# Performance work log

Hardware: AMD Instinct MI355X
Metric: run time of the kernel (lower is better)

The kernel has to match this reference:

```python
import jax, jax.numpy as jnp
import numpy as np

EPS = 1e-12  # matches torch F.normalize eps

def _l2norm(v, axis):
    n = jnp.linalg.norm(v, axis=axis, keepdims=True)
    return v / jnp.maximum(n, EPS)

def setup_inputs() -> dict:
    key = jax.random.key(0)
    k1, k2 = jax.random.split(key)
    x = jax.random.normal(k1, (16, 512, 64, 64), dtype=jnp.float32)
    mem = jax.random.normal(k2, (1024, 512), dtype=jnp.float32)
    memory = _l2norm(mem, axis=1)  # buffer initialized normalized, as in __init__
    return {"x": x, "memory": memory}

def reference(x, memory):
    B, C, H, W = x.shape
    feat = x.transpose(0, 2, 3, 1).reshape(-1, C)          # [N, C], N=B*H*W
    feat_norm = _l2norm(feat, axis=1)                       # [N, C]
    mem_norm = _l2norm(memory, axis=1)                      # [K, C]
    sim = feat_norm @ mem_norm.T                            # [N, K] cosine sims
    attn = jax.nn.softmax(sim, axis=1)                      # [N, K]
    recon = attn @ mem_norm                                 # [N, C]
    recon = recon.reshape(B, H, W, C).transpose(0, 3, 1, 2) # [B, C, H, W]
    match_map = attn.max(axis=1).reshape(B, H, W)           # [B, H, W]
    return recon, match_map
```

## Files before the change

kernel.cpp:

```cpp
#include <hip/hip_runtime.h>

#define C_DIM 512
#define K_MEM 1024

typedef __attribute__((ext_vector_type(8))) short short8;
typedef __attribute__((ext_vector_type(4))) float f32x4;
typedef __attribute__((ext_vector_type(16))) float f32x16;
typedef __attribute__((ext_vector_type(4))) unsigned int u32x4;

#define LGKM0()  asm volatile("s_waitcnt lgkmcnt(0)" ::: "memory")
#define VM0()    asm volatile("s_waitcnt vmcnt(0)" ::: "memory")
#define BAR()    { asm volatile("" ::: "memory"); __builtin_amdgcn_s_barrier(); asm volatile("" ::: "memory"); }
#define SCHED0() __builtin_amdgcn_sched_barrier(0)

#define GLOAD16(dst, addr, imm) \
    asm volatile("global_load_dwordx4 %0, %1, off offset:%c2" \
                 : "=v"(dst) : "v"(addr), "n"(imm))
#define WAITV(N) do { asm volatile("s_waitcnt vmcnt(%c0)" :: "n"(N) : "memory"); \
                      __builtin_amdgcn_sched_barrier(0); } while (0)

__device__ __forceinline__ unsigned short f2bf(float f) {
    unsigned int u = __builtin_bit_cast(unsigned int, f);
    unsigned int r = (u + 0x7fffu + ((u >> 16) & 1u)) >> 16;
    return (unsigned short)r;
}

__device__ __forceinline__ f32x4 mfma16(short8 a, short8 b, f32x4 c) {
    return __builtin_amdgcn_mfma_f32_16x16x32_bf16(a, b, c, 0, 0, 0);
}
__device__ __forceinline__ f32x16 mfma32(short8 a, short8 b, f32x16 c) {
    return __builtin_amdgcn_mfma_f32_32x32x16_bf16(a, b, c, 0, 0, 0);
}

__device__ __forceinline__ void gl_lds16(const void* g, void* l) {
    __builtin_amdgcn_global_load_lds(
        (const __attribute__((address_space(1))) unsigned int*)g,
        (__attribute__((address_space(3))) unsigned int*)l, 16, 0, 0);
}

__global__ __launch_bounds__(256)
void prep_norm(const float* __restrict__ mem, unsigned short* __restrict__ Mn) {
    int k = blockIdx.x, t = threadIdx.x;
    const float* row = mem + (size_t)k * C_DIM;
    float2 v = *reinterpret_cast<const float2*>(row + 2 * t);
    float ss = v.x * v.x + v.y * v.y;
#pragma unroll
    for (int off = 32; off >= 1; off >>= 1) ss += __shfl_xor(ss, off);
    __shared__ float wp[4];
    if ((t & 63) == 0) wp[t >> 6] = ss;
    __syncthreads();
    float tot = wp[0] + wp[1] + wp[2] + wp[3];
    float rn = 1.0f / fmaxf(sqrtf(tot), 1e-12f);
    unsigned int pk = (unsigned int)f2bf(v.x * rn) | ((unsigned int)f2bf(v.y * rn) << 16);
    *reinterpret_cast<unsigned int*>(Mn + (size_t)k * C_DIM + 2 * t) = pk;
}

__global__ __launch_bounds__(256)
void prep_transpose(const unsigned short* __restrict__ Mn, unsigned short* __restrict__ MnT) {
    __shared__ unsigned short tl[64][72];
    int t = threadIdx.x;
    int bk = blockIdx.x & 15, bc = blockIdx.x >> 4;
    int k0 = bk * 64, c0 = bc * 64;
    {
        int kr = t >> 2, gc = (t & 3) * 16;
        const u32x4* src = reinterpret_cast<const u32x4*>(Mn + (size_t)(k0 + kr) * C_DIM + c0 + gc);
        u32x4 a = src[0], b = src[1];
        *reinterpret_cast<u32x4*>(&tl[kr][gc]) = a;
        *reinterpret_cast<u32x4*>(&tl[kr][gc + 8]) = b;
    }
    __syncthreads();
    {
        int cr = t >> 2, gk = (t & 3) * 16;
        unsigned int ow[8];
#pragma unroll
        for (int j = 0; j < 8; ++j)
            ow[j] = (unsigned int)tl[gk + 2 * j][cr] | ((unsigned int)tl[gk + 2 * j + 1][cr] << 16);
        unsigned int* dst = reinterpret_cast<unsigned int*>(MnT + (size_t)(c0 + cr) * K_MEM + k0 + gk);
#pragma unroll
        for (int j = 0; j < 8; ++j) dst[j] = ow[j];
    }
}

__global__ __launch_bounds__(512)
void normx_kernel(const float* __restrict__ x, unsigned short* __restrict__ Fn) {
    __shared__ alignas(16) char FnB[65536];
    __shared__ float normpart[64][9];
    __shared__ float rnormS[64];
    const int t = threadIdx.x, bid = blockIdx.x;
    const int b = bid >> 6, h = bid & 63;
    const int lane = t & 63, wv = t >> 6;
    const int w = lane, cg = wv;
    const float* xp = x + (size_t)b * 2097152 + (size_t)(cg * 64) * 4096 + (size_t)h * 64 + w;
    float xv[64];
#pragma unroll
    for (int i = 0; i < 64; ++i) xv[i] = xp[(size_t)i * 4096];
    float ss = 0.f;
#pragma unroll
    for (int i = 0; i < 64; ++i) ss += xv[i] * xv[i];
    normpart[w][cg] = ss;
    __syncthreads();
    if (t < 64) {
        float s = 0.f;
#pragma unroll
        for (int j = 0; j < 8; ++j) s += normpart[t][j];
        rnormS[t] = 1.0f / fmaxf(sqrtf(s), 1e-12f);
    }
    __syncthreads();
    float rn = rnormS[w];
    char* fnrow = FnB + w * 1024;
#pragma unroll
    for (int j = 0; j < 8; ++j) {
        u32x4 pk4;
#pragma unroll
        for (int p = 0; p < 4; ++p) {
            float v0 = xv[j * 8 + 2 * p] * rn;
            float v1 = xv[j * 8 + 2 * p + 1] * rn;
            pk4[p] = (unsigned int)f2bf(v0) | ((unsigned int)f2bf(v1) << 16);
        }
        int gs = (cg * 8 + j) ^ (w & 31);
        *(u32x4*)(fnrow + (gs << 4)) = pk4;
    }
    __syncthreads();
    const int r = t >> 3;
    char* orow = (char*)(Fn + (size_t)(bid * 64 + r) * C_DIM);
#pragma unroll
    for (int p = 0; p < 8; ++p) {
        int gl = p * 8 + (t & 7);
        u32x4 v = *(const u32x4*)(FnB + r * 1024 + ((gl ^ (r & 31)) << 4));
        *(u32x4*)(orow + gl * 16) = v;
    }
}

__device__ __forceinline__ void stage64(const char* g0, int rowBytes, int kcol,
                                        char* ldsChunk, int j, int wv, int lane) {
    const int rloc = wv * 8 + (lane >> 3);
    const int rglob = j * 64 + rloc;
    const int gs = (lane & 7) ^ (rloc & 7);
    gl_lds16(g0 + (size_t)rglob * rowBytes + kcol + gs * 16, ldsChunk + wv * 1024);
}
#define FRAG(base, r, gk) (*(const short8*)((base) + (r) * 128 + ((((gk)) ^ ((r) & 7)) << 4)))

#define GEMM_KLOOP(NKT, ABYT, BBYT)                                                   \
    {                                                                                  \
        for (int j = 0; j < 4; ++j) stage64(Ag, ABYT, 0, LDSU + j * 8192, j, wv, lane); \
        for (int j = 0; j < 4; ++j) stage64(Bg, BBYT, 0, LDSU + 32768 + j * 8192, j, wv, lane); \
        VM0(); BAR();                                                                   \
    }                                                                                  \
    _Pragma("unroll 1")                                                                \
    for (int kt = 0; kt < (NKT); ++kt) {                                               \
        char* Asp = LDSU + (kt & 1) * 65536;                                           \
        char* Bsp = Asp + 32768;                                                       \
        char* Asn = LDSU + ((kt + 1) & 1) * 65536;                                     \
        char* Bsn = Asn + 32768;                                                       \
        const int kcoln = (kt + 1) * 128;                                              \
        _Pragma("unroll")                                                              \
        for (int s = 0; s < 2; ++s) {                                                  \
            short8 af[4], bfv[4];                                                      \
            if (s == 0 && kt + 1 < (NKT)) {                                            \
                _Pragma("unroll")                                                      \
                for (int j = 0; j < 4; ++j)                                            \
                    stage64(Ag, ABYT, kcoln, Asn + j * 8192, j, wv, lane);             \
            }                                                                          \
            _Pragma("unroll")                                                          \
            for (int i = 0; i < 4; ++i) bfv[i] = FRAG(Bsp, wn * 64 + i * 16 + l15, s * 4 + l4); \
            _Pragma("unroll")                                                          \
            for (int i = 0; i < 4; ++i) af[i] = FRAG(Asp, wm * 128 + i * 16 + l15, s * 4 + l4); \
            SCHED0();                                                                  \
            __builtin_amdgcn_s_setprio(1);                                             \
            _Pragma("unroll")                                                          \
            for (int mf = 0; mf < 4; ++mf)                                             \
                _Pragma("unroll")                                                      \
                for (int nf = 0; nf < 4; ++nf)                                         \
                    acc[mf][nf] = mfma16(af[mf], bfv[nf], acc[mf][nf]);                \
            __builtin_amdgcn_s_setprio(0);                                             \
            SCHED0();                                                                  \
            if (s == 0 && kt + 1 < (NKT)) {                                            \
                _Pragma("unroll")                                                      \
                for (int j = 0; j < 4; ++j)                                            \
                    stage64(Bg, BBYT, kcoln, Bsn + j * 8192, j, wv, lane);             \
            }                                                                          \
            _Pragma("unroll")                                                          \
            for (int i = 0; i < 4; ++i) af[i] = FRAG(Asp, wm * 128 + (4 + i) * 16 + l15, s * 4 + l4); \
            SCHED0();                                                                  \
            __builtin_amdgcn_s_setprio(1);                                             \
            _Pragma("unroll")                                                          \
            for (int mf = 0; mf < 4; ++mf)                                             \
                _Pragma("unroll")                                                      \
                for (int nf = 0; nf < 4; ++nf)                                         \
                    acc[4 + mf][nf] = mfma16(af[mf], bfv[nf], acc[4 + mf][nf]);        \
            __builtin_amdgcn_s_setprio(0);                                             \
            SCHED0();                                                                  \
        }                                                                              \
        if (kt + 1 < (NKT)) VM0();                                                     \
        BAR();                                                                         \
    }

__global__ __launch_bounds__(512)
__attribute__((amdgpu_waves_per_eu(2, 2)))
void gemm1_kernel(const unsigned short* __restrict__ Fn, const unsigned short* __restrict__ Mn,
                  unsigned short* __restrict__ P, float* __restrict__ Zp, float* __restrict__ Mp) {
    __shared__ alignas(16) char LDSU[135168];
    __shared__ float zS[256][4], zM[256][4];

    const int wg = (blockIdx.x & 7) * 128 + (blockIdx.x >> 3);
    const int mt = wg >> 2, ntile = wg & 3;
    const int m0 = mt * 256, n0 = ntile * 256;
    const int t = threadIdx.x, lane = t & 63, wv = t >> 6;
    const int wm = wv >> 2, wn = wv & 3;
    const int l15 = lane & 15, l4 = lane >> 4;

    const char* Ag = (const char*)Fn + (size_t)m0 * 1024;
    const char* Bg = (const char*)Mn + (size_t)n0 * 1024;

    f32x4 acc[8][4];
#pragma unroll
    for (int i = 0; i < 8; ++i)
#pragma unroll
        for (int j = 0; j < 4; ++j) acc[i][j] = (f32x4){0.f, 0.f, 0.f, 0.f};

    GEMM_KLOOP(8, 1024, 1024)

    char* Pscr = LDSU;
#pragma unroll
    for (int mf = 0; mf < 8; ++mf) {
        float zs[4] = {0.f, 0.f, 0.f, 0.f};
        float zm[4] = {0.f, 0.f, 0.f, 0.f};
#pragma unroll
        for (int nf = 0; nf < 4; ++nf) {
            const int col = wn * 64 + nf * 16 + l15;
#pragma unroll
            for (int r = 0; r < 4; ++r) {
                float e = __expf(acc[mf][nf][r]);
                zs[r] += e;
                zm[r] = fmaxf(zm[r], e);
                const int row = wm * 128 + mf * 16 + l4 * 4 + r;
                *(unsigned short*)(Pscr + row * 528 + col * 2) = f2bf(e);
            }
        }
#pragma unroll
        for (int off = 1; off < 16; off <<= 1)
#pragma unroll
            for (int r = 0; r < 4; ++r) {
                zs[r] += __shfl_xor(zs[r], off);
                zm[r] = fmaxf(zm[r], __shfl_xor(zm[r], off));
            }
        if (l15 == 0) {
#pragma unroll
            for (int r = 0; r < 4; ++r) {
                const int row = wm * 128 + mf * 16 + l4 * 4 + r;
                zS[row][wn] = zs[r];
                zM[row][wn] = zm[r];
            }
        }
    }
    LGKM0(); BAR();
    if (t < 256) {
        float zq = zS[t][0] + zS[t][1] + zS[t][2] + zS[t][3];
        float mq = fmaxf(fmaxf(zM[t][0], zM[t][1]), fmaxf(zM[t][2], zM[t][3]));
        Zp[(size_t)(m0 + t) * 4 + ntile] = zq;
        Mp[(size_t)(m0 + t) * 4 + ntile] = mq;
    }
#pragma unroll
    for (int p = 0; p < 8; ++p) {
        const int r = p * 32 + (t >> 4);
        const char* src = Pscr + r * 528 + (t & 15) * 32;
        char* dst = (char*)P + (size_t)(m0 + r) * 2048 + n0 * 2 + (t & 15) * 32;
        u32x4 v0 = *(const u32x4*)src;
        u32x4 v1 = *(const u32x4*)(src + 16);
        *(u32x4*)dst = v0;
        *(u32x4*)(dst + 16) = v1;
    }
}

__global__ __launch_bounds__(256)
void stats_kernel(const float* __restrict__ Zp, const float* __restrict__ Mp,
                  float* __restrict__ Zinv, float* __restrict__ match) {
    int i = blockIdx.x * 256 + threadIdx.x;
    f32x4 a = *(const f32x4*)(Zp + (size_t)i * 4);
    f32x4 c = *(const f32x4*)(Mp + (size_t)i * 4);
    float s = a[0] + a[1] + a[2] + a[3];
    float m = fmaxf(fmaxf(c[0], c[1]), fmaxf(c[2], c[3]));
    float zi = 1.0f / s;
    Zinv[i] = zi;
    match[i] = m * zi;
}

__global__ __launch_bounds__(512)
__attribute__((amdgpu_waves_per_eu(2, 2)))
void gemm2_kernel(const unsigned short* __restrict__ P, const unsigned short* __restrict__ MnT,
                  const float* __restrict__ Zinv, float* __restrict__ recon) {
    __shared__ alignas(16) char LDSU[131072];
    __shared__ float zinvS[256];

    const int wg = (blockIdx.x & 7) * 64 + (blockIdx.x >> 3);
    const int mt = wg >> 1, ntile = wg & 1;
    const int m0 = mt * 256, n0 = ntile * 256;
    const int t = threadIdx.x, lane = t & 63, wv = t >> 6;
    const int wm = wv >> 2, wn = wv & 3;
    const int l15 = lane & 15, l4 = lane >> 4;

    if (t < 256) zinvS[t] = Zinv[m0 + t];

    const char* Ag = (const char*)P + (size_t)m0 * 2048;
    const char* Bg = (const char*)MnT + (size_t)n0 * 2048;

    f32x4 acc[8][4];
#pragma unroll
    for (int i = 0; i < 8; ++i)
#pragma unroll
        for (int j = 0; j < 4; ++j) acc[i][j] = (f32x4){0.f, 0.f, 0.f, 0.f};

    GEMM_KLOOP(16, 2048, 2048)

    const int b = m0 >> 12;
    const int inb0 = m0 & 4095;
#pragma unroll
    for (int mf = 0; mf < 8; ++mf) {
        f32x4 zv = *(const f32x4*)(&zinvS[wm * 128 + mf * 16 + l4 * 4]);
#pragma unroll
        for (int nf = 0; nf < 4; ++nf) {
            f32x4 v = acc[mf][nf];
            v[0] *= zv[0]; v[1] *= zv[1]; v[2] *= zv[2]; v[3] *= zv[3];
            const int c = n0 + wn * 64 + nf * 16 + l15;
            const int inb = inb0 + wm * 128 + mf * 16 + l4 * 4;
            *(f32x4*)(recon + (size_t)b * 2097152 + (size_t)c * 4096 + inb) = v;
        }
    }
}

__global__ __launch_bounds__(512)
__attribute__((amdgpu_waves_per_eu(2, 2)))
void fused_attn(const float* __restrict__ x,
                const unsigned short* __restrict__ Mn,
                const unsigned short* __restrict__ MnT,
                float* __restrict__ recon,
                float* __restrict__ match) {
    __shared__ alignas(16) char FnB[65536];
    __shared__ alignas(16) char PldsB[2 * 32768];
    __shared__ float Zinv[64], rnormS[64];

    const int t = threadIdx.x;
    const int bid = blockIdx.x;
    const int b = bid >> 6, h = bid & 63;
    const int lane = t & 63, wv = t >> 6;
    const int l31 = lane & 31, l5 = lane >> 5;
    const int ko = wv;
    const int cb = wv * 64;

    {
        float* normpart = (float*)PldsB;
        const int w = lane, cg = wv;
        const float* xp = x + (size_t)b * 2097152 + (size_t)(cg * 64) * 4096 + (size_t)h * 64 + w;
        float xv[64];
#pragma unroll
        for (int i = 0; i < 64; ++i) xv[i] = xp[(size_t)i * 4096];
        float ss = 0.f;
#pragma unroll
        for (int i = 0; i < 64; ++i) ss += xv[i] * xv[i];
        normpart[w * 9 + cg] = ss;
        __syncthreads();
        if (t < 64) {
            float s = 0.f;
#pragma unroll
            for (int j = 0; j < 8; ++j) s += normpart[t * 9 + j];
            rnormS[t] = 1.0f / fmaxf(sqrtf(s), 1e-12f);
        }
        __syncthreads();
        float rn = rnormS[w];
        char* fnrow = FnB + w * 1024;
#pragma unroll
        for (int j = 0; j < 8; ++j) {
            u32x4 pk4;
#pragma unroll
            for (int p = 0; p < 4; ++p) {
                float v0 = xv[j * 8 + 2 * p] * rn;
                float v1 = xv[j * 8 + 2 * p + 1] * rn;
                pk4[p] = (unsigned int)f2bf(v0) | ((unsigned int)f2bf(v1) << 16);
            }
            int gs = (cg * 8 + j) ^ (w & 31);
            *(u32x4*)(fnrow + (gs << 4)) = pk4;
        }
    }
    __syncthreads();

    f32x16 acc3[2][2];
#pragma unroll
    for (int i = 0; i < 2; ++i)
#pragma unroll
        for (int j = 0; j < 2; ++j)
#pragma unroll
            for (int r = 0; r < 16; ++r) acc3[i][j][r] = 0.f;

    float regZ[2] = {0.f, 0.f};
    float regM[2] = {-3.0e38f, -3.0e38f};
    const char* fnR0 = FnB + l31 * 1024;
    const char* fnR1 = FnB + (32 + l31) * 1024;

#pragma unroll 1
    for (int kt = 0; kt < 4; ++kt) {
        const char* aG = (const char*)Mn + ((size_t)(kt * 256 + ko * 32 + l31) << 10) + (l5 << 4);
        u32x4 afb[2][4];
        GLOAD16(afb[0][0], aG, 0);
        GLOAD16(afb[0][1], aG, 32);
        GLOAD16(afb[0][2], aG, 64);
        GLOAD16(afb[0][3], aG, 96);
        f32x16 acc1[2];
#pragma unroll
        for (int j = 0; j < 2; ++j)
#pragma unroll
            for (int r = 0; r < 16; ++r) acc1[j][r] = 0.f;
#pragma unroll
        for (int g = 0; g < 8; ++g) {
            if (g < 7) {
#pragma unroll
                for (int s = 0; s < 4; ++s)
                    GLOAD16(afb[(g + 1) & 1][s], aG, ((g + 1) * 4 + s) * 32);
                WAITV(4);
            } else {
                WAITV(0);
            }
#pragma unroll
            for (int s = 0; s < 4; ++s) {
                const int st = g * 4 + s;
                const int gsw = (((st << 1) | l5) ^ l31) << 4;
                short8 b0 = *(const short8*)(fnR0 + gsw);
                short8 b1 = *(const short8*)(fnR1 + gsw);
                short8 av = __builtin_bit_cast(short8, afb[g & 1][s]);
                acc1[0] = mfma32(av, b0, acc1[0]);
                acc1[1] = mfma32(av, b1, acc1[1]);
            }
        }
        const char* aG2a = (const char*)MnT + ((size_t)(cb + l31) << 11) + ((size_t)kt << 9) + (l5 << 4);
        const char* aG2b = aG2a + 65536;
        u32x4 a2b[2][4];
        GLOAD16(a2b[0][0], aG2a, 0);
        GLOAD16(a2b[0][1], aG2b, 0);
        GLOAD16(a2b[0][2], aG2a, 32);
        GLOAD16(a2b[0][3], aG2b, 32);
        unsigned int P32[2][8];
#pragma unroll
        for (int nt = 0; nt < 2; ++nt) {
            float s0 = 0.f, m0 = -3.0e38f;
#pragma unroll
            for (int j = 0; j < 8; ++j) {
                float a0 = acc1[nt][2 * j], a1 = acc1[nt][2 * j + 1];
                m0 = fmaxf(m0, fmaxf(a0, a1));
                float e0 = __expf(a0), e1 = __expf(a1);
                P32[nt][j] = (unsigned int)f2bf(e0) | ((unsigned int)f2bf(e1) << 16);
                s0 += e0 + e1;
            }
            s0 += __shfl_xor(s0, 32);
            m0 = fmaxf(m0, __shfl_xor(m0, 32));
            regZ[nt] += s0;
            regM[nt] = fmaxf(regM[nt], m0);
        }
        char* Pb = PldsB + (kt & 1) * 32768;
#pragma unroll
        for (int nt = 0; nt < 2; ++nt) {
            const int n = nt * 32 + l31;
            char* prow = Pb + n * 512;
#pragma unroll
            for (int jp = 0; jp < 4; ++jp) {
                const int gk = ko * 4 + jp;
                uint2 v;
                v.x = P32[nt][2 * jp];
                v.y = P32[nt][2 * jp + 1];
                *(uint2*)(prow + ((gk ^ (n & 31)) << 4) + 8 * l5) = v;
            }
        }
        LGKM0(); BAR();
#pragma unroll
        for (int g = 0; g < 8; ++g) {
            if (g < 7) {
#pragma unroll
                for (int u = 0; u < 2; ++u) {
                    GLOAD16(a2b[(g + 1) & 1][u * 2 + 0], aG2a, ((g + 1) * 2 + u) * 32);
                    GLOAD16(a2b[(g + 1) & 1][u * 2 + 1], aG2b, ((g + 1) * 2 + u) * 32);
                }
                WAITV(4);
            } else {
                WAITV(0);
            }
#pragma unroll
            for (int u = 0; u < 2; ++u) {
                const int ks = g * 2 + u;
                const int gsw = (((ks << 1) | l5) ^ l31) << 4;
                short8 bp0 = *(const short8*)(Pb + l31 * 512 + gsw);
                short8 bp1 = *(const short8*)(Pb + (32 + l31) * 512 + gsw);
                short8 a0 = __builtin_bit_cast(short8, a2b[g & 1][u * 2 + 0]);
                short8 a1 = __builtin_bit_cast(short8, a2b[g & 1][u * 2 + 1]);
                acc3[0][0] = mfma32(a0, bp0, acc3[0][0]);
                acc3[0][1] = mfma32(a0, bp1, acc3[0][1]);
                acc3[1][0] = mfma32(a1, bp0, acc3[1][0]);
                acc3[1][1] = mfma32(a1, bp1, acc3[1][1]);
            }
        }
    }
    {
        float* pS = (float*)FnB;
        float* pM = (float*)(FnB + 2048);
        if (l5 == 0) {
            pS[ko * 64 + l31] = regZ[0];
            pS[ko * 64 + 32 + l31] = regZ[1];
            pM[ko * 64 + l31] = regM[0];
            pM[ko * 64 + 32 + l31] = regM[1];
        }
        LGKM0(); BAR();
        if (t < 64) {
            float s = 0.f, m = -3.0e38f;
#pragma unroll
            for (int k8 = 0; k8 < 8; ++k8) {
                s += pS[k8 * 64 + t];
                m = fmaxf(m, pM[k8 * 64 + t]);
            }
            float zi = 1.0f / s;
            Zinv[t] = zi;
            match[(size_t)bid * 64 + t] = __expf(m) * zi;
        }
        LGKM0(); BAR();
    }
    const float zi0 = Zinv[l31], zi1 = Zinv[32 + l31];
    float* rbase = recon + (size_t)b * 2097152 + (size_t)h * 64;
#pragma unroll
    for (int ct = 0; ct < 2; ++ct) {
#pragma unroll
        for (int r = 0; r < 16; ++r) {
            const int c = cb + ct * 32 + (r & 3) + 8 * (r >> 2) + 4 * l5;
            float* rp = rbase + (size_t)c * 4096;
            rp[l31] = acc3[ct][0][r] * zi0;
            rp[32 + l31] = acc3[ct][1][r] * zi1;
        }
    }
}

extern "C" void kernel_launch(void* const* d_in, const int* in_sizes, int n_in,
                              void* d_out, int out_size, void* d_ws, size_t ws_size,
                              hipStream_t stream) {
    (void)in_sizes; (void)n_in; (void)out_size;
    if (ws_size < (size_t)2 * 1024 * 1024) return;

    const float* x = (const float*)d_in[0];
    const float* mem = (const float*)d_in[1];
    float* recon = (float*)d_out;
    float* match = recon + (size_t)16 * 512 * 64 * 64;
    char* ws = (char*)d_ws;
    unsigned short* Mn = (unsigned short*)ws;
    unsigned short* MnT = (unsigned short*)(ws + 1048576);

    prep_norm<<<dim3(K_MEM), dim3(256), 0, stream>>>(mem, Mn);
    prep_transpose<<<dim3(128), dim3(256), 0, stream>>>(Mn, MnT);

    const size_t NEED = 205783040ull;
    if (ws_size >= NEED) {
        unsigned short* Fn = (unsigned short*)(ws + 2097152);
        unsigned short* P  = (unsigned short*)(ws + 69206016);
        float* Zp = (float*)(ws + 203423744);
        float* Mp = (float*)(ws + 204472320);
        float* Zi = (float*)(ws + 205520896);
        normx_kernel<<<dim3(1024), dim3(512), 0, stream>>>(x, Fn);
        gemm1_kernel<<<dim3(1024), dim3(512), 0, stream>>>(Fn, Mn, P, Zp, Mp);
        stats_kernel<<<dim3(256), dim3(256), 0, stream>>>(Zp, Mp, Zi, match);
        gemm2_kernel<<<dim3(512), dim3(512), 0, stream>>>(P, MnT, Zi, recon);
    } else {
        fused_attn<<<dim3(1024), dim3(512), 0, stream>>>(x, Mn, MnT, recon, match);
    }
}
```

Before: 276.7 us.

## Restructure GEMM k-loop into half-tile staged pipeline with partial vmcnt waits

```diff
diff --git a/kernel.cpp b/kernel.cpp
--- a/kernel.cpp
+++ b/kernel.cpp
@@ -131,69 +131,80 @@
     }
 }
 
-__device__ __forceinline__ void stage64(const char* g0, int rowBytes, int kcol,
-                                        char* ldsChunk, int j, int wv, int lane) {
-    const int rloc = wv * 8 + (lane >> 3);
-    const int rglob = j * 64 + rloc;
-    const int gs = (lane & 7) ^ (rloc & 7);
-    gl_lds16(g0 + (size_t)rglob * rowBytes + kcol + gs * 16, ldsChunk + wv * 1024);
-}
-#define FRAG(base, r, gk) (*(const short8*)((base) + (r) * 128 + ((((gk)) ^ ((r) & 7)) << 4)))
-
-#define GEMM_KLOOP(NKT, ABYT, BBYT)                                                   \
-    {                                                                                  \
-        for (int j = 0; j < 4; ++j) stage64(Ag, ABYT, 0, LDSU + j * 8192, j, wv, lane); \
-        for (int j = 0; j < 4; ++j) stage64(Bg, BBYT, 0, LDSU + 32768 + j * 8192, j, wv, lane); \
-        VM0(); BAR();                                                                   \
-    }                                                                                  \
-    _Pragma("unroll 1")                                                                \
-    for (int kt = 0; kt < (NKT); ++kt) {                                               \
-        char* Asp = LDSU + (kt & 1) * 65536;                                           \
-        char* Bsp = Asp + 32768;                                                       \
-        char* Asn = LDSU + ((kt + 1) & 1) * 65536;                                     \
-        char* Bsn = Asn + 32768;                                                       \
-        const int kcoln = (kt + 1) * 128;                                              \
-        _Pragma("unroll")                                                              \
-        for (int s = 0; s < 2; ++s) {                                                  \
-            short8 af[4], bfv[4];                                                      \
-            if (s == 0 && kt + 1 < (NKT)) {                                            \
-                _Pragma("unroll")                                                      \
-                for (int j = 0; j < 4; ++j)                                            \
-                    stage64(Ag, ABYT, kcoln, Asn + j * 8192, j, wv, lane);             \
-            }                                                                          \
-            _Pragma("unroll")                                                          \
-            for (int i = 0; i < 4; ++i) bfv[i] = FRAG(Bsp, wn * 64 + i * 16 + l15, s * 4 + l4); \
-            _Pragma("unroll")                                                          \
-            for (int i = 0; i < 4; ++i) af[i] = FRAG(Asp, wm * 128 + i * 16 + l15, s * 4 + l4); \
-            SCHED0();                                                                  \
-            __builtin_amdgcn_s_setprio(1);                                             \
-            _Pragma("unroll")                                                          \
-            for (int mf = 0; mf < 4; ++mf)                                             \
-                _Pragma("unroll")                                                      \
-                for (int nf = 0; nf < 4; ++nf)                                         \
-                    acc[mf][nf] = mfma16(af[mf], bfv[nf], acc[mf][nf]);                \
-            __builtin_amdgcn_s_setprio(0);                                             \
-            SCHED0();                                                                  \
-            if (s == 0 && kt + 1 < (NKT)) {                                            \
-                _Pragma("unroll")                                                      \
-                for (int j = 0; j < 4; ++j)                                            \
-                    stage64(Bg, BBYT, kcoln, Bsn + j * 8192, j, wv, lane);             \
-            }                                                                          \
-            _Pragma("unroll")                                                          \
-            for (int i = 0; i < 4; ++i) af[i] = FRAG(Asp, wm * 128 + (4 + i) * 16 + l15, s * 4 + l4); \
-            SCHED0();                                                                  \
-            __builtin_amdgcn_s_setprio(1);                                             \
-            _Pragma("unroll")                                                          \
-            for (int mf = 0; mf < 4; ++mf)                                             \
-                _Pragma("unroll")                                                      \
-                for (int nf = 0; nf < 4; ++nf)                                         \
-                    acc[4 + mf][nf] = mfma16(af[mf], bfv[nf], acc[4 + mf][nf]);        \
-            __builtin_amdgcn_s_setprio(0);                                             \
-            SCHED0();                                                                  \
-        }                                                                              \
-        if (kt + 1 < (NKT)) VM0();                                                     \
-        BAR();                                                                         \
-    }
+__device__ __forceinline__ void stage_half(const char* g0, int rowBytes, int kcol,
+                                           char* halfBuf, int wv, int lane) {
+    const int gsrc = (lane & 3) ^ ((lane >> 2) & 3) ^ ((lane >> 4) & 3);
+#pragma unroll
+    for (int j = 0; j < 2; ++j) {
+        const int r = j * 128 + wv * 16 + (lane >> 2);
+        gl_lds16(g0 + (size_t)r * rowBytes + kcol + gsrc * 16, halfBuf + j * 8192 + wv * 1024);
+    }
+}
+
+#define FRAGH(base, r, g) \
+    (*(const short8*)((base) + (size_t)(r) * 64 + ((((g) ^ ((r) & 3) ^ (((r) >> 2) & 3))) << 4)))
+
+__device__ __forceinline__ void read_frags(short8 (&af)[4], short8 (&bf)[4],
+                                           const char* Ah, const char* Bh,
+                                           int arow0, int brow0, int l15, int l4) {
+#pragma unroll
+    for (int i = 0; i < 4; ++i) {
+        af[i] = FRAGH(Ah, arow0 + i * 16 + l15, l4);
+        bf[i] = FRAGH(Bh, brow0 + i * 16 + l15, l4);
+    }
+}
+
+__device__ __forceinline__ void mm16(f32x4 (&acc)[8][4], int base,
+                                     const short8 (&af)[4], const short8 (&bf)[4]) {
+    __builtin_amdgcn_s_setprio(1);
+#pragma unroll
+    for (int mf = 0; mf < 4; ++mf)
+#pragma unroll
+        for (int nf = 0; nf < 4; ++nf)
+            acc[base + mf][nf] = mfma16(af[mf], bf[nf], acc[base + mf][nf]);
+    __builtin_amdgcn_s_setprio(0);
+}
+
+template <int NKT>
+__device__ __forceinline__ void kloop8(const char* Ag, int abyt, const char* Bg, int bbyt,
+                                       char* LDSU, f32x4 (&acc)[8][4],
+                                       int wv, int lane, int wm, int wn, int l15, int l4) {
+    stage_half(Ag, abyt, 0, LDSU + 0, wv, lane);
+    stage_half(Bg, bbyt, 0, LDSU + 32768, wv, lane);
+    stage_half(Ag, abyt, 64, LDSU + 16384, wv, lane);
+    stage_half(Bg, bbyt, 64, LDSU + 49152, wv, lane);
+    WAITV(4); BAR();
+#pragma unroll 1
+    for (int kt = 0; kt < NKT; ++kt) {
+        char* base = LDSU + (kt & 1) * 65536;
+        char* nbase = LDSU + ((kt + 1) & 1) * 65536;
+        const int kb = (kt + 1) * 128;
+        const bool more = (kt + 1) < NKT;
+        short8 af[4], bf[4];
+        read_frags(af, bf, base, base + 32768, wm * 128, wn * 64, l15, l4);
+        if (more) stage_half(Ag, abyt, kb, nbase, wv, lane);
+        BAR(); LGKM0(); SCHED0();
+        mm16(acc, 0, af, bf);
+        BAR();
+        read_frags(af, bf, base, base + 32768, wm * 128 + 64, wn * 64, l15, l4);
+        if (more) stage_half(Bg, bbyt, kb, nbase + 32768, wv, lane);
+        BAR(); LGKM0(); SCHED0();
+        mm16(acc, 4, af, bf);
+        if (more) { WAITV(4); } else { WAITV(0); }
+        BAR();
+        read_frags(af, bf, base + 16384, base + 49152, wm * 128, wn * 64, l15, l4);
+        if (more) stage_half(Ag, abyt, kb + 64, nbase + 16384, wv, lane);
+        BAR(); LGKM0(); SCHED0();
+        mm16(acc, 0, af, bf);
+        BAR();
+        read_frags(af, bf, base + 16384, base + 49152, wm * 128 + 64, wn * 64, l15, l4);
+        if (more) stage_half(Bg, bbyt, kb + 64, nbase + 49152, wv, lane);
+        BAR(); LGKM0(); SCHED0();
+        mm16(acc, 4, af, bf);
+        if (more) { WAITV(4); } else { WAITV(0); }
+        BAR();
+    }
+}
 
 __global__ __launch_bounds__(512)
 __attribute__((amdgpu_waves_per_eu(2, 2)))
@@ -218,7 +229,7 @@
 #pragma unroll
         for (int j = 0; j < 4; ++j) acc[i][j] = (f32x4){0.f, 0.f, 0.f, 0.f};
 
-    GEMM_KLOOP(8, 1024, 1024)
+    kloop8<8>(Ag, 1024, Bg, 1024, LDSU, acc, wv, lane, wm, wn, l15, l4);
 
     char* Pscr = LDSU;
 #pragma unroll
@@ -310,7 +321,7 @@
 #pragma unroll
         for (int j = 0; j < 4; ++j) acc[i][j] = (f32x4){0.f, 0.f, 0.f, 0.f};
 
-    GEMM_KLOOP(16, 2048, 2048)
+    kloop8<16>(Ag, 2048, Bg, 2048, LDSU, acc, wv, lane, wm, wn, l15, l4);
 
     const int b = m0 >> 12;
     const int inb0 = m0 & 4095;
```

Result: no change. 277.1 us (+0.1%).
